# Performance work log

Hardware: AMD Instinct MI355X
Metric: run time of the kernel (lower is better)

## Reference

```python
import jax, jax.numpy as jnp
import numpy as np
import math

B, C, H, W = 32, 256, 56, 56
M = 16            # num_frequency_mixtures
MIX = 4           # sqrt(M)
K = 8             # num_fourier_basis + 1
HID = 16
STRIDE = (1, 1)
EPS = 1e-5


def setup_inputs() -> dict:
    key = jax.random.key(0)
    ks = jax.random.split(key, 8)
    return {
        "x": jax.random.normal(ks[0], (B, C, H, W), jnp.float32),
        "fc1_w": jax.random.normal(ks[1], (HID, C), jnp.float32) * 0.08,
        "fc1_b": jnp.zeros((HID,), jnp.float32),
        "ln_g": jnp.ones((HID,), jnp.float32),
        "ln_b": jnp.zeros((HID,), jnp.float32),
        "fh_w": jax.random.normal(ks[2], (C * M * K, HID), jnp.float32) * 0.08,
        "fh_b": jnp.zeros((C * M * K,), jnp.float32),
        "basis_real": jax.random.normal(ks[3], (K, 56, 32), jnp.float32) * 0.5,
        "basis_imag": jax.random.normal(ks[4], (K, 56, 32), jnp.float32) * 0.5,
        "conv_w": jax.random.normal(ks[5], (C, C), jnp.float32) * (1.0 / math.sqrt(C)),
        "bn_g": jnp.ones((C,), jnp.float32),
        "bn_b": jnp.zeros((C,), jnp.float32),
    }


def reference(x, fc1_w, fc1_b, ln_g, ln_b, fh_w, fh_b,
              basis_real, basis_imag, conv_w, bn_g, bn_b):
    b, c, h, w = x.shape
    # --- FrequencyAttention: GAP -> fc1 -> LN -> ReLU -> fourier_head ---
    ctx = x.mean(axis=(2, 3))                          # (B, C)
    hdn = ctx @ fc1_w.T + fc1_b                        # (B, HID)
    mu = hdn.mean(-1, keepdims=True)
    var = hdn.var(-1, keepdims=True)
    hdn = (hdn - mu) / jnp.sqrt(var + EPS) * ln_g + ln_b
    hdn = jax.nn.relu(hdn)
    att = hdn @ fh_w.T + fh_b                          # (B, C*M*K)

    coeffs = jax.nn.softmax(att.reshape(b, c, M, K), axis=-1)  # (B,C,M,K)

    # --- work-canvas sizes ---
    h_out, w_out = h // STRIDE[0], w // STRIDE[1]
    h_work = math.ceil(h / MIX) * MIX                  # 56
    w_f = w // 2 + 1                                   # 29
    w_f_work = math.ceil(w_f / MIX) * MIX              # 32
    w_work = (w_f_work - 1) * 2 if w_f_work > 1 else 1 # 62

    if (h_work, w_work) != (h, w):
        x_work = jax.image.resize(x, (b, c, h_work, w_work), "bilinear")
    else:
        x_work = x

    x_ft = jnp.fft.rfft2(x_work, s=(h_work, w_work), norm="ortho")  # (B,C,Hw,Wfw) complex
    wf = x_ft.shape[-1]                                # == w_f_work
    ph, pwf = h_work // MIX, wf // MIX                 # 14, 8

    basis = jax.lax.complex(basis_real, basis_imag)    # (K, Hw, Wfw)
    basis_p = basis.reshape(K, MIX, ph, MIX, pwf).transpose(1, 3, 0, 2, 4)
    basis_p = basis_p.reshape(M, K, ph, pwf)           # (M,K,ph,pwf)

    x_ft_p = x_ft.reshape(b, c, MIX, ph, MIX, pwf).transpose(0, 2, 4, 1, 3, 5)
    x_ft_p = x_ft_p.reshape(b, M, c, ph, pwf)          # (B,M,C,ph,pwf)

    coeffs_c = jax.lax.complex(coeffs, jnp.zeros_like(coeffs))
    coeffs_p = coeffs_c.transpose(0, 2, 1, 3)          # (B,M,C,K)

    kernel = jnp.einsum("bmck,mkhw->bmchw", coeffs_p, basis_p)  # (B,M,C,ph,pwf)
    out_ft_p = x_ft_p * kernel

    out_ft = out_ft_p.reshape(b, MIX, MIX, c, ph, pwf).transpose(0, 3, 1, 4, 2, 5)
    out_ft = out_ft.reshape(b, c, h_work, wf)

    s_work = (h_work // STRIDE[0], w_work // STRIDE[1])
    y = jnp.fft.irfft2(out_ft, s=s_work, norm="ortho")  # (B,C,56,62)

    if y.shape[2:] != (h_out, w_out):
        y = jax.image.resize(y, (b, c, h_out, w_out), "bilinear")

    # --- 1x1 conv + BatchNorm (batch statistics, training-mode math) ---
    y = jnp.einsum("bchw,oc->bohw", y, conv_w)
    m = y.mean(axis=(0, 2, 3))
    v = y.var(axis=(0, 2, 3))
    y = (y - m[None, :, None, None]) / jnp.sqrt(v + EPS)[None, :, None, None]
    y = y * bn_g[None, :, None, None] + bn_b[None, :, None, None]
    return y
```

## Files before the change

kernel.cpp:

```cpp
#include <hip/hip_runtime.h>
#include <math.h>

typedef __attribute__((ext_vector_type(4))) float f32x4;
typedef __attribute__((ext_vector_type(8))) short s16x8;
typedef __attribute__((ext_vector_type(4))) short s16x4;
typedef unsigned short ushort_t;

#define MFMA16(a, b, c) __builtin_amdgcn_mfma_f32_16x16x32_bf16((a), (b), (c), 0, 0, 0)

#define WO_CTX    0u
#define WO_HDN    32768u
#define WO_BNSUM  34816u
#define WO_BNSQ   35840u
#define WO_SCALE  36864u
#define WO_SHIFT  37888u
#define WO_COEF   40960u
#define WO_BMT_H  4235264u
#define WO_BMT_L  4243456u
#define WO_FARE_H 4251648u
#define WO_FARE_L 4268032u
#define WO_FAIM_H 4284416u
#define WO_FAIM_L 4300800u
#define WO_FDRE_H 4317184u
#define WO_FDRE_L 4333568u
#define WO_FDIM_H 4349952u
#define WO_FDIM_L 4366336u
#define WO_DTT_H  4382720u
#define WO_DTT_L  4390912u
#define WO_CW_H   4399104u
#define WO_CW_L   4530176u
#define WO_YBF    4661248u

__device__ __forceinline__ ushort_t f2bf(float f) {
  unsigned int u = __builtin_bit_cast(unsigned int, f);
  unsigned int r = (u + 0x7fffu + ((u >> 16) & 1u)) >> 16;
  return (ushort_t)r;
}
__device__ __forceinline__ float bf2f(ushort_t h) {
  unsigned int u = ((unsigned int)h) << 16;
  return __builtin_bit_cast(float, u);
}

__device__ double bmat_val(int w, int vv) {
  const int v = vv & 31;
  const bool isI = vv >= 32;
  double accR = 0.0, accI = 0.0;
  for (int wp = 0; wp < 62; ++wp) {
    const double src = (wp + 0.5) * (56.0 / 62.0) - 0.5;
    const int w0 = (int)floor(src);
    const double f = src - (double)w0;
    const double s0 = (w0 >= 0 && w0 <= 55) ? (1.0 - f) : 0.0;
    const double s1 = (w0 + 1 >= 0 && w0 + 1 <= 55) ? f : 0.0;
    const double ssum = s0 + s1;
    double wgt = 0.0;
    if (w == w0) wgt = s0 / ssum;
    else if (w == w0 + 1) wgt = s1 / ssum;
    if (wgt != 0.0) {
      const int p = (v * wp) % 62;
      const double ang = 6.283185307179586476925286766559 * (double)p / 62.0;
      accR += wgt * cos(ang);
      accI -= wgt * sin(ang);
    }
  }
  const double nrm = 1.0 / sqrt(3472.0);
  return (isI ? accI : accR) * nrm;
}

__device__ double dt_component(int v, bool isI, int wq) {
  const double ks = 62.0 / 56.0;
  const double src = (wq + 0.5) * ks - 0.5;
  double wsum = 0.0;
  for (int wp = 0; wp < 62; ++wp) {
    const double xx = fabs(src - (double)wp) / ks;
    if (xx < 1.0) wsum += 1.0 - xx;
  }
  const double cv = (v == 0 || v == 31) ? 1.0 : 2.0;
  double accR = 0.0, accI = 0.0;
  for (int wp = 0; wp < 62; ++wp) {
    const double xx = fabs(src - (double)wp) / ks;
    if (xx >= 1.0) continue;
    const double wgt = (1.0 - xx) / wsum;
    double cc, ss;
    if (v == 0)       { cc = 1.0; ss = 0.0; }
    else if (v == 31) { cc = (wp & 1) ? -1.0 : 1.0; ss = 0.0; }
    else {
      const int p = (v * wp) % 62;
      const double ang = 6.283185307179586476925286766559 * (double)p / 62.0;
      cc = cos(ang); ss = sin(ang);
    }
    accR += wgt * cv * cc;
    accI -= wgt * cv * ss;
  }
  const double nrm = 1.0 / sqrt(3472.0);
  return (isI ? accI : accR) * nrm;
}

__device__ __forceinline__ void emit_hilo(ushort_t* hp, ushort_t* lp, int off, double val) {
  const float fv = (float)val;
  const ushort_t h = f2bf(fv);
  const float hf = bf2f(h);
  const ushort_t l = f2bf((float)(val - (double)hf));
  hp[off] = h;
  lp[off] = l;
}

__global__ void k_const(const float* __restrict__ conv_w,
                        ushort_t* BmT_h, ushort_t* BmT_l,
                        ushort_t* FARe_h, ushort_t* FARe_l,
                        ushort_t* FAIm_h, ushort_t* FAIm_l,
                        ushort_t* FDRe_h, ushort_t* FDRe_l,
                        ushort_t* FDIm_h, ushort_t* FDIm_l,
                        ushort_t* DtT_h, ushort_t* DtT_l,
                        ushort_t* W_h, ushort_t* W_l) {
  const int idx = blockIdx.x * 256 + threadIdx.x;
  if (idx < 4096) {
    const int vv = idx >> 6, k = idx & 63;
    const double v = (k < 56) ? bmat_val(k, vv) : 0.0;
    emit_hilo(BmT_h, BmT_l, idx, v);
  } else if (idx < 36864) {
    const int t = (idx - 4096) & 8191;
    const int which = (idx - 4096) >> 13;
    const int row = t >> 7, k = t & 127;
    double val = 0.0;
    if (row < 56 && k < 112) {
      const int h = (k < 56) ? k : k - 56;
      const double ang = 6.283185307179586476925286766559 *
                         (double)((row * h) % 56) / 56.0;
      const double c = cos(ang), s = sin(ang);
      const bool lowk = (k < 56);
      if (which == 0)      val = lowk ? c : s;
      else if (which == 1) val = lowk ? -s : c;
      else if (which == 2) val = lowk ? c : -s;
      else                 val = lowk ? s : c;
    }
    ushort_t* hp = (which == 0) ? FARe_h : (which == 1) ? FAIm_h : (which == 2) ? FDRe_h : FDIm_h;
    ushort_t* lp = (which == 0) ? FARe_l : (which == 1) ? FAIm_l : (which == 2) ? FDRe_l : FDIm_l;
    emit_hilo(hp, lp, t, val);
  } else if (idx < 40960) {
    const int t = idx - 36864;
    const int w = t >> 6, kk = t & 63;
    const double val = (w < 56) ? dt_component(kk >> 1, (kk & 1) != 0, w) : 0.0;
    emit_hilo(DtT_h, DtT_l, t, val);
  } else if (idx < 106496) {
    const int t = idx - 40960;
    emit_hilo(W_h, W_l, t, (double)conv_w[t]);
  }
}

__global__ __launch_bounds__(256) void k_gap(const float* __restrict__ x,
                                             float* __restrict__ ctx) {
  const int img = blockIdx.x;
  const int tid = threadIdx.x;
  const float4* p4 = (const float4*)(x + (size_t)img * 3136);
  float s = 0.f;
  for (int i = tid; i < 784; i += 256) {
    const float4 v = p4[i];
    s += v.x + v.y + v.z + v.w;
  }
  for (int off = 32; off > 0; off >>= 1) s += __shfl_down(s, off, 64);
  __shared__ float ls[4];
  if ((tid & 63) == 0) ls[tid >> 6] = s;
  __syncthreads();
  if (tid == 0) ctx[img] = (ls[0] + ls[1] + ls[2] + ls[3]) * (1.0f / 3136.0f);
}

__global__ void k_mlp(const float* __restrict__ ctx, const float* __restrict__ fc1_w,
                      const float* __restrict__ fc1_b, const float* __restrict__ ln_g,
                      const float* __restrict__ ln_b, float* __restrict__ hdn) {
  const int b = blockIdx.x;
  const int j = threadIdx.x;
  __shared__ float h[16];
  if (j < 16) {
    const float* cr = ctx + b * 256;
    const float* wr = fc1_w + j * 256;
    float acc = fc1_b[j];
    for (int c0 = 0; c0 < 256; ++c0) acc = fmaf(cr[c0], wr[c0], acc);
    h[j] = acc;
  }
  __syncthreads();
  if (j < 16) {
    float mu = 0.f, m2 = 0.f;
    for (int t = 0; t < 16; ++t) { mu += h[t]; m2 += h[t] * h[t]; }
    mu *= 0.0625f; m2 *= 0.0625f;
    const float var = m2 - mu * mu;
    const float val = (h[j] - mu) / sqrtf(var + 1e-5f) * ln_g[j] + ln_b[j];
    hdn[b * 16 + j] = fmaxf(val, 0.f);
  }
}

__global__ __launch_bounds__(256) void k_coeffs(const float* __restrict__ hdn,
                                                const float* __restrict__ fh_w,
                                                const float* __restrict__ fh_b,
                                                float* __restrict__ coeffs) {
  const int gid = blockIdx.x * 256 + threadIdx.x;
  const int b = gid >> 12;
  const int cm = gid & 4095;
  float hv[16];
  const float* hp = hdn + b * 16;
#pragma unroll
  for (int j = 0; j < 16; ++j) hv[j] = hp[j];
  const int row0 = cm * 8;
  float a[8];
  float mx = -1e30f;
#pragma unroll
  for (int k = 0; k < 8; ++k) {
    const float* wr = fh_w + (size_t)(row0 + k) * 16;
    float acc = fh_b[row0 + k];
#pragma unroll
    for (int j = 0; j < 16; ++j) acc = fmaf(hv[j], wr[j], acc);
    a[k] = acc;
    mx = fmaxf(mx, acc);
  }
  float s = 0.f;
#pragma unroll
  for (int k = 0; k < 8; ++k) { a[k] = expf(a[k] - mx); s += a[k]; }
  const float inv = 1.f / s;
  float* outp = coeffs + (size_t)gid * 8;
#pragma unroll
  for (int k = 0; k < 8; ++k) outp[k] = a[k] * inv;
}

__global__ __launch_bounds__(256) void k_fft(
    const float* __restrict__ x, const float* __restrict__ coeffs,
    const float* __restrict__ basR, const float* __restrict__ basI,
    const ushort_t* __restrict__ BmT_h, const ushort_t* __restrict__ BmT_l,
    const ushort_t* __restrict__ FARe_h, const ushort_t* __restrict__ FARe_l,
    const ushort_t* __restrict__ FAIm_h, const ushort_t* __restrict__ FAIm_l,
    const ushort_t* __restrict__ FDRe_h, const ushort_t* __restrict__ FDRe_l,
    const ushort_t* __restrict__ FDIm_h, const ushort_t* __restrict__ FDIm_l,
    const ushort_t* __restrict__ DtT_h, const ushort_t* __restrict__ DtT_l,
    ushort_t* __restrict__ ybf) {
  __shared__ __align__(16) ushort_t xta[64 * 72];
  __shared__ __align__(16) ushort_t x1T[32 * 136];
  __shared__ __align__(16) ushort_t x2T[32 * 136];
  __shared__ float gf[3584];
  const int img = blockIdx.x;
  const int tid = threadIdx.x;
  const int wave = tid >> 6, lane = tid & 63, col = lane & 15, quad = lane >> 4;
  const f32x4 zf = {0.f, 0.f, 0.f, 0.f};

  for (int i = tid; i < 224; i += 256) {
    const int h = i >> 2, c = i & 3;
    *(unsigned int*)&xta[h * 72 + 56 + c * 2] = 0u;
  }
  for (int i = tid; i < 512; i += 256) {
    const int r = (i >> 3) & 31, c = i & 7;
    ushort_t* bp = (i < 256) ? x1T : x2T;
    *(unsigned int*)&bp[r * 136 + 112 + c * 2] = 0u;
  }
  {
    const float4* xp = (const float4*)(x + (size_t)img * 3136);
    for (int f = tid; f < 784; f += 256) {
      const float4 v = xp[f];
      const int h = f / 14, w4 = (f % 14) * 4;
      s16x4 p;
      p[0] = (short)f2bf(v.x); p[1] = (short)f2bf(v.y);
      p[2] = (short)f2bf(v.z); p[3] = (short)f2bf(v.w);
      *(s16x4*)&xta[h * 72 + w4] = p;
    }
    const float* co = coeffs + (size_t)img * 128;
    for (int q = tid; q < 1792; q += 256) {
      const int u = q >> 5, v = q & 31;
      const int m = (u / 14) * 4 + (v >> 3);
      const float* cm = co + m * 8;
      float gr = 0.f, gi = 0.f;
#pragma unroll
      for (int k = 0; k < 8; ++k) {
        gr = fmaf(cm[k], basR[k * 1792 + q], gr);
        gi = fmaf(cm[k], basI[k * 1792 + q], gi);
      }
      gf[q] = gr;
      gf[1792 + q] = gi;
    }
  }
  __syncthreads();

  {
    const int mt = wave;
    const int arow = (mt * 16 + col) * 72;
    const s16x8 a0 = *(const s16x8*)&xta[arow + quad * 8];
    const s16x8 a1 = *(const s16x8*)&xta[arow + 32 + quad * 8];
    const int h0 = mt * 16 + quad * 4;
    for (int nt = 0; nt < 4; ++nt) {
      const int nrow = nt * 16 + col;
      const s16x8 bh0 = *(const s16x8*)&BmT_h[nrow * 64 + quad * 8];
      const s16x8 bl0 = *(const s16x8*)&BmT_l[nrow * 64 + quad * 8];
      const s16x8 bh1 = *(const s16x8*)&BmT_h[nrow * 64 + 32 + quad * 8];
      const s16x8 bl1 = *(const s16x8*)&BmT_l[nrow * 64 + 32 + quad * 8];
      f32x4 acc = zf;
      acc = MFMA16(a0, bh0, acc);
      acc = MFMA16(a0, bl0, acc);
      acc = MFMA16(a1, bh1, acc);
      acc = MFMA16(a1, bl1, acc);
      if (h0 < 56) {
        s16x4 p;
        p[0] = (short)f2bf(acc[0]); p[1] = (short)f2bf(acc[1]);
        p[2] = (short)f2bf(acc[2]); p[3] = (short)f2bf(acc[3]);
        const int vr = nrow & 31;
        const int kk = (nrow < 32) ? h0 : 56 + h0;
        *(s16x4*)&x1T[vr * 136 + kk] = p;
      }
    }
  }
  __syncthreads();

  {
    const int mt = wave;
    f32x4 accRe[2] = {zf, zf}, accIm[2] = {zf, zf};
    for (int ks = 0; ks < 4; ++ks) {
      const int aoff = (mt * 16 + col) * 128 + ks * 32 + quad * 8;
      const s16x8 aRh = *(const s16x8*)&FARe_h[aoff];
      const s16x8 aRl = *(const s16x8*)&FARe_l[aoff];
      const s16x8 aIh = *(const s16x8*)&FAIm_h[aoff];
      const s16x8 aIl = *(const s16x8*)&FAIm_l[aoff];
#pragma unroll
      for (int nt = 0; nt < 2; ++nt) {
        const s16x8 b = *(const s16x8*)&x1T[(nt * 16 + col) * 136 + ks * 32 + quad * 8];
        accRe[nt] = MFMA16(aRh, b, accRe[nt]);
        accRe[nt] = MFMA16(aRl, b, accRe[nt]);
        accIm[nt] = MFMA16(aIh, b, accIm[nt]);
        accIm[nt] = MFMA16(aIl, b, accIm[nt]);
      }
    }
    const int u0 = mt * 16 + quad * 4;
    if (u0 < 56) {
#pragma unroll
      for (int nt = 0; nt < 2; ++nt) {
        const int v = nt * 16 + col;
        s16x4 pR, pI;
#pragma unroll
        for (int r = 0; r < 4; ++r) {
          const int u = u0 + r;
          const float gr = gf[u * 32 + v];
          const float gi = gf[1792 + u * 32 + v];
          const float re = accRe[nt][r] * gr - accIm[nt][r] * gi;
          const float im = accRe[nt][r] * gi + accIm[nt][r] * gr;
          pR[r] = (short)f2bf(re);
          pI[r] = (short)f2bf(im);
        }
        *(s16x4*)&x2T[v * 136 + u0] = pR;
        *(s16x4*)&x2T[v * 136 + 56 + u0] = pI;
      }
    }
  }
  __syncthreads();

  {
    const int mt = wave;
    f32x4 accRe[2] = {zf, zf}, accIm[2] = {zf, zf};
    for (int ks = 0; ks < 4; ++ks) {
      const int aoff = (mt * 16 + col) * 128 + ks * 32 + quad * 8;
      const s16x8 aRh = *(const s16x8*)&FDRe_h[aoff];
      const s16x8 aRl = *(const s16x8*)&FDRe_l[aoff];
      const s16x8 aIh = *(const s16x8*)&FDIm_h[aoff];
      const s16x8 aIl = *(const s16x8*)&FDIm_l[aoff];
#pragma unroll
      for (int nt = 0; nt < 2; ++nt) {
        const s16x8 b = *(const s16x8*)&x2T[(nt * 16 + col) * 136 + ks * 32 + quad * 8];
        accRe[nt] = MFMA16(aRh, b, accRe[nt]);
        accRe[nt] = MFMA16(aRl, b, accRe[nt]);
        accIm[nt] = MFMA16(aIh, b, accIm[nt]);
        accIm[nt] = MFMA16(aIl, b, accIm[nt]);
      }
    }
    const int h0 = mt * 16 + quad * 4;
#pragma unroll
    for (int nt = 0; nt < 2; ++nt) {
      const int v = nt * 16 + col;
#pragma unroll
      for (int r = 0; r < 4; ++r) {
        const unsigned int pk = (unsigned int)f2bf(accRe[nt][r]) |
                                ((unsigned int)f2bf(accIm[nt][r]) << 16);
        *(unsigned int*)&xta[(h0 + r) * 72 + 2 * v] = pk;
      }
    }
  }
  __syncthreads();

  {
    const int mt = wave;
    const int arow = (mt * 16 + col) * 72;
    const s16x8 a0 = *(const s16x8*)&xta[arow + quad * 8];
    const s16x8 a1 = *(const s16x8*)&xta[arow + 32 + quad * 8];
    const int h0 = mt * 16 + quad * 4;
    ushort_t* yo = ybf + (size_t)img * 3136;
    for (int nt = 0; nt < 4; ++nt) {
      const int w = nt * 16 + col;
      const s16x8 bh0 = *(const s16x8*)&DtT_h[w * 64 + quad * 8];
      const s16x8 bl0 = *(const s16x8*)&DtT_l[w * 64 + quad * 8];
      const s16x8 bh1 = *(const s16x8*)&DtT_h[w * 64 + 32 + quad * 8];
      const s16x8 bl1 = *(const s16x8*)&DtT_l[w * 64 + 32 + quad * 8];
      f32x4 acc = zf;
      acc = MFMA16(a0, bh0, acc);
      acc = MFMA16(a0, bl0, acc);
      acc = MFMA16(a1, bh1, acc);
      acc = MFMA16(a1, bl1, acc);
      if (h0 < 56 && w < 56) {
#pragma unroll
        for (int r = 0; r < 4; ++r) yo[(h0 + r) * 56 + w] = f2bf(acc[r]);
      }
    }
  }
}

__global__ __launch_bounds__(256) void k_conv(const ushort_t* __restrict__ ybf,
                                              const ushort_t* __restrict__ W_h,
                                              const ushort_t* __restrict__ W_l,
                                              float* __restrict__ z) {
  const int pb = blockIdx.x;
  const int oh = blockIdx.y;
  const int b = blockIdx.z;
  const int tid = threadIdx.x;
  const int wave = tid >> 6, lane = tid & 63, col = lane & 15, quad = lane >> 4;
  const f32x4 zf = {0.f, 0.f, 0.f, 0.f};
  f32x4 acc[8][4];
#pragma unroll
  for (int mt = 0; mt < 8; ++mt)
#pragma unroll
    for (int i = 0; i < 4; ++i) acc[mt][i] = zf;

  const size_t ybase = (size_t)b * 256 * 3136;
  int p0i[4];
  bool act[4];
#pragma unroll
  for (int i = 0; i < 4; ++i) {
    p0i[i] = pb * 256 + (wave * 4 + i) * 16;
    act[i] = p0i[i] < 3136;
  }

  for (int ks = 0; ks < 8; ++ks) {
    const int c0 = ks * 32 + quad * 8;
    s16x8 bfr[4];
#pragma unroll
    for (int i = 0; i < 4; ++i) {
      if (act[i]) {
        s16x8 t;
#pragma unroll
        for (int j = 0; j < 8; ++j)
          t[j] = (short)ybf[ybase + (size_t)(c0 + j) * 3136 + p0i[i] + col];
        bfr[i] = t;
      }
    }
#pragma unroll
    for (int mt = 0; mt < 8; ++mt) {
      const int orow = oh * 128 + mt * 16 + col;
      const s16x8 ah = *(const s16x8*)&W_h[orow * 256 + ks * 32 + quad * 8];
      const s16x8 al = *(const s16x8*)&W_l[orow * 256 + ks * 32 + quad * 8];
#pragma unroll
      for (int i = 0; i < 4; ++i) {
        if (act[i]) {
          acc[mt][i] = MFMA16(ah, bfr[i], acc[mt][i]);
          acc[mt][i] = MFMA16(al, bfr[i], acc[mt][i]);
        }
      }
    }
  }

#pragma unroll
  for (int mt = 0; mt < 8; ++mt) {
#pragma unroll
    for (int i = 0; i < 4; ++i) {
      if (!act[i]) continue;
#pragma unroll
      for (int r = 0; r < 4; ++r) {
        const int o = oh * 128 + mt * 16 + quad * 4 + r;
        z[((size_t)b * 256 + o) * 3136 + p0i[i] + col] = acc[mt][i][r];
      }
    }
  }
}

__global__ __launch_bounds__(256) void k_bnsum(const float* __restrict__ z,
                                               float* __restrict__ bnsum,
                                               float* __restrict__ bnsq) {
  const int bo = blockIdx.x;
  const int tid = threadIdx.x;
  const float4* p4 = (const float4*)(z + (size_t)bo * 3136);
  float s = 0.f, s2 = 0.f;
  for (int i = tid; i < 784; i += 256) {
    const float4 v = p4[i];
    s += v.x + v.y + v.z + v.w;
    s2 += v.x * v.x + v.y * v.y + v.z * v.z + v.w * v.w;
  }
  for (int off = 32; off > 0; off >>= 1) {
    s += __shfl_down(s, off, 64);
    s2 += __shfl_down(s2, off, 64);
  }
  __shared__ float ls[8];
  if ((tid & 63) == 0) { ls[tid >> 6] = s; ls[4 + (tid >> 6)] = s2; }
  __syncthreads();
  if (tid == 0) {
    atomicAdd(bnsum + (bo & 255), ls[0] + ls[1] + ls[2] + ls[3]);
    atomicAdd(bnsq + (bo & 255), ls[4] + ls[5] + ls[6] + ls[7]);
  }
}

__global__ void k_bnstats(const float* __restrict__ bnsum, const float* __restrict__ bnsq,
                          const float* __restrict__ bn_g, const float* __restrict__ bn_b,
                          float* __restrict__ scale, float* __restrict__ shift) {
  const int o = threadIdx.x;
  if (o < 256) {
    const float N = 32.f * 3136.f;
    const float m = bnsum[o] / N;
    const float v = bnsq[o] / N - m * m;
    const float sc = bn_g[o] / sqrtf(v + 1e-5f);
    scale[o] = sc;
    shift[o] = bn_b[o] - m * sc;
  }
}

__global__ __launch_bounds__(256) void k_bnapply(float* __restrict__ z,
                                                 const float* __restrict__ scale,
                                                 const float* __restrict__ shift) {
  const size_t i = ((size_t)blockIdx.x * 256 + threadIdx.x) * 4;
  const int ch = (int)((i / 3136) & 255);
  const float sc = scale[ch], sh = shift[ch];
  float4 v = *(float4*)(z + i);
  v.x = fmaf(v.x, sc, sh);
  v.y = fmaf(v.y, sc, sh);
  v.z = fmaf(v.z, sc, sh);
  v.w = fmaf(v.w, sc, sh);
  *(float4*)(z + i) = v;
}

extern "C" void kernel_launch(void* const* d_in, const int* in_sizes, int n_in,
                              void* d_out, int out_size, void* d_ws, size_t ws_size,
                              hipStream_t stream) {
  const float* x          = (const float*)d_in[0];
  const float* fc1_w      = (const float*)d_in[1];
  const float* fc1_b      = (const float*)d_in[2];
  const float* ln_g       = (const float*)d_in[3];
  const float* ln_b       = (const float*)d_in[4];
  const float* fh_w       = (const float*)d_in[5];
  const float* fh_b       = (const float*)d_in[6];
  const float* basis_real = (const float*)d_in[7];
  const float* basis_imag = (const float*)d_in[8];
  const float* conv_w     = (const float*)d_in[9];
  const float* bn_g       = (const float*)d_in[10];
  const float* bn_b       = (const float*)d_in[11];
  float* out = (float*)d_out;
  char* ws = (char*)d_ws;
  (void)in_sizes; (void)n_in; (void)out_size; (void)ws_size;

  float* ctx   = (float*)(ws + WO_CTX);
  float* hdn   = (float*)(ws + WO_HDN);
  float* bnsum = (float*)(ws + WO_BNSUM);
  float* bnsq  = (float*)(ws + WO_BNSQ);
  float* scale = (float*)(ws + WO_SCALE);
  float* shift = (float*)(ws + WO_SHIFT);
  float* coef  = (float*)(ws + WO_COEF);
  ushort_t* BmT_h  = (ushort_t*)(ws + WO_BMT_H);
  ushort_t* BmT_l  = (ushort_t*)(ws + WO_BMT_L);
  ushort_t* FARe_h = (ushort_t*)(ws + WO_FARE_H);
  ushort_t* FARe_l = (ushort_t*)(ws + WO_FARE_L);
  ushort_t* FAIm_h = (ushort_t*)(ws + WO_FAIM_H);
  ushort_t* FAIm_l = (ushort_t*)(ws + WO_FAIM_L);
  ushort_t* FDRe_h = (ushort_t*)(ws + WO_FDRE_H);
  ushort_t* FDRe_l = (ushort_t*)(ws + WO_FDRE_L);
  ushort_t* FDIm_h = (ushort_t*)(ws + WO_FDIM_H);
  ushort_t* FDIm_l = (ushort_t*)(ws + WO_FDIM_L);
  ushort_t* DtT_h  = (ushort_t*)(ws + WO_DTT_H);
  ushort_t* DtT_l  = (ushort_t*)(ws + WO_DTT_L);
  ushort_t* W_h    = (ushort_t*)(ws + WO_CW_H);
  ushort_t* W_l    = (ushort_t*)(ws + WO_CW_L);
  ushort_t* ybf    = (ushort_t*)(ws + WO_YBF);

  hipMemsetAsync(bnsum, 0, 2048, stream);

  hipLaunchKernelGGL(k_const, dim3(416), dim3(256), 0, stream,
                     conv_w, BmT_h, BmT_l, FARe_h, FARe_l, FAIm_h, FAIm_l,
                     FDRe_h, FDRe_l, FDIm_h, FDIm_l, DtT_h, DtT_l, W_h, W_l);
  hipLaunchKernelGGL(k_gap, dim3(8192), dim3(256), 0, stream, x, ctx);
  hipLaunchKernelGGL(k_mlp, dim3(32), dim3(64), 0, stream,
                     ctx, fc1_w, fc1_b, ln_g, ln_b, hdn);
  hipLaunchKernelGGL(k_coeffs, dim3(512), dim3(256), 0, stream, hdn, fh_w, fh_b, coef);
  hipLaunchKernelGGL(k_fft, dim3(8192), dim3(256), 0, stream,
                     x, coef, basis_real, basis_imag,
                     BmT_h, BmT_l, FARe_h, FARe_l, FAIm_h, FAIm_l,
                     FDRe_h, FDRe_l, FDIm_h, FDIm_l, DtT_h, DtT_l, ybf);
  hipLaunchKernelGGL(k_conv, dim3(13, 2, 32), dim3(256), 0, stream, ybf, W_h, W_l, out);
  hipLaunchKernelGGL(k_bnsum, dim3(8192), dim3(256), 0, stream, out, bnsum, bnsq);
  hipLaunchKernelGGL(k_bnstats, dim3(1), dim3(256), 0, stream,
                     bnsum, bnsq, bn_g, bn_b, scale, shift);
  hipLaunchKernelGGL(k_bnapply, dim3(25088), dim3(256), 0, stream, out, scale, shift);
}
```

Measured before the change: 705.5 us.

## Fuse BN statistics into conv kernel with LDS-staged, double-buffered input tiles

The 1x1 conv kernel now computes all 256 output channels per block over 128 pixels. It stages the bf16 activations through a swizzled, double-buffered LDS tile with register prefetch instead of doing strided scalar global gathers. The BatchNorm sum and sum-of-squares reduction now runs in the conv epilogue through shuffles, LDS atomics and global atomics, which removes the separate k_bnsum pass that re-read the whole output. Nontemporal stores are used for the ybf and z outputs, which may hurt if later kernels want those lines still in cache.

```diff
diff --git a/kernel.cpp b/kernel.cpp
--- a/kernel.cpp
+++ b/kernel.cpp
@@ -397,7 +397,8 @@
       acc = MFMA16(a1, bl1, acc);
       if (h0 < 56 && w < 56) {
 #pragma unroll
-        for (int r = 0; r < 4; ++r) yo[(h0 + r) * 56 + w] = f2bf(acc[r]);
+        for (int r = 0; r < 4; ++r)
+          __builtin_nontemporal_store(f2bf(acc[r]), &yo[(h0 + r) * 56 + w]);
       }
     }
   }
@@ -406,93 +407,127 @@
 __global__ __launch_bounds__(256) void k_conv(const ushort_t* __restrict__ ybf,
                                               const ushort_t* __restrict__ W_h,
                                               const ushort_t* __restrict__ W_l,
-                                              float* __restrict__ z) {
+                                              float* __restrict__ z,
+                                              float* __restrict__ bnsum,
+                                              float* __restrict__ bnsq) {
+  __shared__ __align__(16) ushort_t tile[2 * 32 * 136];
+  __shared__ float ls_sum[256];
+  __shared__ float ls_sq[256];
   const int pb = blockIdx.x;
-  const int oh = blockIdx.y;
-  const int b = blockIdx.z;
+  const int b  = blockIdx.y;
   const int tid = threadIdx.x;
   const int wave = tid >> 6, lane = tid & 63, col = lane & 15, quad = lane >> 4;
   const f32x4 zf = {0.f, 0.f, 0.f, 0.f};
-  f32x4 acc[8][4];
-#pragma unroll
-  for (int mt = 0; mt < 8; ++mt)
-#pragma unroll
-    for (int i = 0; i < 4; ++i) acc[mt][i] = zf;
-
-  const size_t ybase = (size_t)b * 256 * 3136;
-  int p0i[4];
-  bool act[4];
-#pragma unroll
-  for (int i = 0; i < 4; ++i) {
-    p0i[i] = pb * 256 + (wave * 4 + i) * 16;
-    act[i] = p0i[i] < 3136;
-  }
-
+
+  ls_sum[tid] = 0.f;
+  ls_sq[tid] = 0.f;
+
+  f32x4 acc[16][2];
+#pragma unroll
+  for (int mt = 0; mt < 16; ++mt)
+#pragma unroll
+    for (int i = 0; i < 2; ++i) acc[mt][i] = zf;
+
+  const int p0 = pb * 128;
+  int pL[2];
+  bool act[2];
+#pragma unroll
+  for (int i = 0; i < 2; ++i) {
+    pL[i] = (wave * 2 + i) * 16;
+    act[i] = (p0 + pL[i]) < 3136;
+  }
+  int psw[2];
+#pragma unroll
+  for (int i = 0; i < 2; ++i) psw[i] = (pL[i] + col) ^ (quad << 3);
+
+  int sc[2], sp8[2], sld[2];
+  bool sact[2];
+#pragma unroll
+  for (int n = 0; n < 2; ++n) {
+    const int ch = n * 256 + tid;
+    const int c = ch >> 4;
+    const int p8 = (ch & 15) * 8;
+    sc[n] = c;
+    sp8[n] = p8;
+    sact[n] = (p0 + p8) < 3136;
+    sld[n] = c * 136 + (p8 ^ (((c >> 3) & 3) << 3));
+  }
+
+  const s16x8 zs = {0, 0, 0, 0, 0, 0, 0, 0};
+  s16x8 pf[2];
+#pragma unroll
+  for (int n = 0; n < 2; ++n)
+    pf[n] = sact[n]
+        ? *(const s16x8*)&ybf[(size_t)(b * 256 + sc[n]) * 3136 + p0 + sp8[n]]
+        : zs;
+
+  int buf = 0;
   for (int ks = 0; ks < 8; ++ks) {
-    const int c0 = ks * 32 + quad * 8;
-    s16x8 bfr[4];
-#pragma unroll
-    for (int i = 0; i < 4; ++i) {
-      if (act[i]) {
-        s16x8 t;
-#pragma unroll
-        for (int j = 0; j < 8; ++j)
-          t[j] = (short)ybf[ybase + (size_t)(c0 + j) * 3136 + p0i[i] + col];
-        bfr[i] = t;
-      }
-    }
-#pragma unroll
-    for (int mt = 0; mt < 8; ++mt) {
-      const int orow = oh * 128 + mt * 16 + col;
+#pragma unroll
+    for (int n = 0; n < 2; ++n)
+      *(s16x8*)&tile[buf * 4352 + sld[n]] = pf[n];
+    __syncthreads();
+    if (ks < 7) {
+#pragma unroll
+      for (int n = 0; n < 2; ++n)
+        pf[n] = sact[n]
+            ? *(const s16x8*)&ybf[(size_t)(b * 256 + (ks + 1) * 32 + sc[n]) * 3136 + p0 + sp8[n]]
+            : zs;
+    }
+    s16x8 bfr[2];
+#pragma unroll
+    for (int i = 0; i < 2; ++i) {
+#pragma unroll
+      for (int j = 0; j < 8; ++j)
+        bfr[i][j] = (short)tile[buf * 4352 + (quad * 8 + j) * 136 + psw[i]];
+    }
+#pragma unroll
+    for (int mt = 0; mt < 16; ++mt) {
+      const int orow = mt * 16 + col;
       const s16x8 ah = *(const s16x8*)&W_h[orow * 256 + ks * 32 + quad * 8];
       const s16x8 al = *(const s16x8*)&W_l[orow * 256 + ks * 32 + quad * 8];
 #pragma unroll
-      for (int i = 0; i < 4; ++i) {
+      for (int i = 0; i < 2; ++i) {
+        acc[mt][i] = MFMA16(ah, bfr[i], acc[mt][i]);
+        acc[mt][i] = MFMA16(al, bfr[i], acc[mt][i]);
+      }
+    }
+    buf ^= 1;
+  }
+
+#pragma unroll
+  for (int mt = 0; mt < 16; ++mt) {
+#pragma unroll
+    for (int r = 0; r < 4; ++r) {
+      const int chn = mt * 16 + quad * 4 + r;
+      float s = 0.f, s2 = 0.f;
+#pragma unroll
+      for (int i = 0; i < 2; ++i) {
         if (act[i]) {
-          acc[mt][i] = MFMA16(ah, bfr[i], acc[mt][i]);
-          acc[mt][i] = MFMA16(al, bfr[i], acc[mt][i]);
+          const float v = acc[mt][i][r];
+          s += v;
+          s2 += v * v;
+          __builtin_nontemporal_store(
+              v, &z[((size_t)b * 256 + chn) * 3136 + p0 + pL[i] + col]);
         }
       }
-    }
-  }
-
-#pragma unroll
-  for (int mt = 0; mt < 8; ++mt) {
-#pragma unroll
-    for (int i = 0; i < 4; ++i) {
-      if (!act[i]) continue;
-#pragma unroll
-      for (int r = 0; r < 4; ++r) {
-        const int o = oh * 128 + mt * 16 + quad * 4 + r;
-        z[((size_t)b * 256 + o) * 3136 + p0i[i] + col] = acc[mt][i][r];
-      }
-    }
-  }
-}
-
-__global__ __launch_bounds__(256) void k_bnsum(const float* __restrict__ z,
-                                               float* __restrict__ bnsum,
-                                               float* __restrict__ bnsq) {
-  const int bo = blockIdx.x;
-  const int tid = threadIdx.x;
-  const float4* p4 = (const float4*)(z + (size_t)bo * 3136);
-  float s = 0.f, s2 = 0.f;
-  for (int i = tid; i < 784; i += 256) {
-    const float4 v = p4[i];
-    s += v.x + v.y + v.z + v.w;
-    s2 += v.x * v.x + v.y * v.y + v.z * v.z + v.w * v.w;
-  }
-  for (int off = 32; off > 0; off >>= 1) {
-    s += __shfl_down(s, off, 64);
-    s2 += __shfl_down(s2, off, 64);
-  }
-  __shared__ float ls[8];
-  if ((tid & 63) == 0) { ls[tid >> 6] = s; ls[4 + (tid >> 6)] = s2; }
+      s += __shfl_xor(s, 8, 16);
+      s += __shfl_xor(s, 4, 16);
+      s += __shfl_xor(s, 2, 16);
+      s += __shfl_xor(s, 1, 16);
+      s2 += __shfl_xor(s2, 8, 16);
+      s2 += __shfl_xor(s2, 4, 16);
+      s2 += __shfl_xor(s2, 2, 16);
+      s2 += __shfl_xor(s2, 1, 16);
+      if (col == 0) {
+        atomicAdd(&ls_sum[chn], s);
+        atomicAdd(&ls_sq[chn], s2);
+      }
+    }
+  }
   __syncthreads();
-  if (tid == 0) {
-    atomicAdd(bnsum + (bo & 255), ls[0] + ls[1] + ls[2] + ls[3]);
-    atomicAdd(bnsq + (bo & 255), ls[4] + ls[5] + ls[6] + ls[7]);
-  }
+  atomicAdd(&bnsum[tid], ls_sum[tid]);
+  atomicAdd(&bnsq[tid], ls_sq[tid]);
 }
 
 __global__ void k_bnstats(const float* __restrict__ bnsum, const float* __restrict__ bnsq,
@@ -578,8 +613,8 @@
                      x, coef, basis_real, basis_imag,
                      BmT_h, BmT_l, FARe_h, FARe_l, FAIm_h, FAIm_l,
                      FDRe_h, FDRe_l, FDIm_h, FDIm_l, DtT_h, DtT_l, ybf);
-  hipLaunchKernelGGL(k_conv, dim3(13, 2, 32), dim3(256), 0, stream, ybf, W_h, W_l, out);
-  hipLaunchKernelGGL(k_bnsum, dim3(8192), dim3(256), 0, stream, out, bnsum, bnsq);
+  hipLaunchKernelGGL(k_conv, dim3(25, 32), dim3(256), 0, stream,
+                     ybf, W_h, W_l, out, bnsum, bnsq);
   hipLaunchKernelGGL(k_bnstats, dim3(1), dim3(256), 0, stream,
                      bnsum, bnsq, bn_g, bn_b, scale, shift);
   hipLaunchKernelGGL(k_bnapply, dim3(25088), dim3(256), 0, stream, out, scale, shift);
```

Measured after the change: 764.7 us. +8.4%, slower.
